# Optimization experiments

Hardware: AMD Instinct MI355X
Metric: run time of the kernel (lower is better)

The kernel has to match this reference:

```python
import jax, jax.numpy as jnp
import numpy as np

N_NODES = 100000
N_EDGES = 1600000
F_IN = 128
HID = 64
N_CLS = 40


def _sage_conv(x, src, dst, Wl, bl, Wr, num_nodes):
    # PyG SAGEConv (aggr='mean', root_weight=True, normalize=False):
    # out = lin_l(mean_{j in N(i)} x_j) + lin_r(x_i)
    msg = x[src]                                              # [E, F] gather
    agg = jax.ops.segment_sum(msg, dst, num_segments=num_nodes)
    deg = jax.ops.segment_sum(jnp.ones_like(dst, dtype=x.dtype), dst,
                              num_segments=num_nodes)
    mean = agg / jnp.maximum(deg, 1.0)[:, None]               # [N, F]
    return mean @ Wl.T + bl + x @ Wr.T


def setup_inputs() -> dict:
    key = jax.random.key(0)
    ks = jax.random.split(key, 16)

    def lin(k, out_d, in_d):
        bound = 1.0 / np.sqrt(in_d)
        return jax.random.uniform(k, (out_d, in_d), jnp.float32, -bound, bound)

    x = jax.random.normal(ks[0], (N_NODES, F_IN), jnp.float32)
    edge_index = jax.random.randint(ks[1], (2, N_EDGES), 0, N_NODES, jnp.int64)

    return {
        "x": x,
        "edge_index": edge_index,
        "W1l": lin(ks[2], HID, F_IN), "b1": jnp.zeros((HID,), jnp.float32),
        "W1r": lin(ks[3], HID, F_IN),
        "W2l": lin(ks[4], HID, HID), "b2": jnp.zeros((HID,), jnp.float32),
        "W2r": lin(ks[5], HID, HID),
        "W3l": lin(ks[6], HID, HID), "b3": jnp.zeros((HID,), jnp.float32),
        "W3r": lin(ks[7], HID, HID),
        "Wout": lin(ks[8], N_CLS, HID),
        "bout": jnp.zeros((N_CLS,), jnp.float32),
    }


def reference(x, edge_index, W1l, b1, W1r, W2l, b2, W2r, W3l, b3, W3r, Wout, bout):
    src, dst = edge_index[0], edge_index[1]
    n = x.shape[0]
    h = _sage_conv(x, src, dst, W1l, b1, W1r, n)
    h = jax.nn.elu(h)
    h = _sage_conv(h, src, dst, W2l, b2, W2r, n)
    h = jax.nn.elu(h)
    h = _sage_conv(h, src, dst, W3l, b3, W3r, n)
    return h @ Wout.T + bout
```

## Files before the change

kernel.cpp:

```cpp
#include <hip/hip_runtime.h>


static inline size_t ws_align(size_t x) { return (x + 511) & ~size_t(511); }

#define MAXBC  104
#define CAPL   96
#define EB_CAP 24576

using frag_ab = __attribute__((ext_vector_type(8))) short;
using f32x4   = __attribute__((ext_vector_type(4))) float;
using us4     = __attribute__((ext_vector_type(4))) unsigned short;

__device__ inline short f2bf(float f) {
    unsigned u = __builtin_bit_cast(unsigned, f);
    u += 0x7fff + ((u >> 16) & 1);
    return (short)(u >> 16);
}
__device__ inline float b2f(unsigned short h) {
    unsigned u = ((unsigned)h) << 16;
    return __builtin_bit_cast(float, u);
}


__global__ void zero_kernel(int* __restrict__ p, int n) {
    int i = blockIdx.x * blockDim.x + threadIdx.x;
    if (i < n) p[i] = 0;
}

__global__ void prep_all(const float* __restrict__ W1l, const float* __restrict__ W1r,
                         const float* __restrict__ W2l, const float* __restrict__ W2r,
                         const float* __restrict__ W3l, const float* __restrict__ W3r,
                         unsigned short* __restrict__ fw) {
    const int idx = blockIdx.x * 256 + threadIdx.x;
    if (idx >= 32768) return;
    const float* W;
    unsigned short* out;
    int F, rel;
    if (idx < 8192)       { W = W1l; out = fw;        F = 128; rel = idx; }
    else if (idx < 16384) { W = W1r; out = fw + 8192; F = 128; rel = idx - 8192; }
    else {
        const int q = (idx - 16384) >> 12;
        rel = (idx - 16384) & 4095;
        F = 64;
        W = (q == 0) ? W2l : (q == 1) ? W2r : (q == 2) ? W3l : W3r;
        out = fw + 16384 + q * 4096;
    }
    const int k = rel % F;
    const int col = rel / F;
    out[(k >> 3) * 512 + col * 8 + (k & 7)] = (unsigned short)f2bf(W[rel]);
}


__global__ void pass1_bin(const int* __restrict__ src, const int* __restrict__ dst,
                          int* __restrict__ bcur, unsigned* __restrict__ ebuf,
                          int nE, int nN, int nbc) {
    __shared__ unsigned lbuf[MAXBC][CAPL];
    __shared__ int bcnt[MAXBC];
    __shared__ int gbase[MAXBC];
    const int t = threadIdx.x;
    const int e0 = blockIdx.x * 4096;
    for (int i = t; i < MAXBC; i += 256) bcnt[i] = 0;
    __syncthreads();
#pragma unroll
    for (int q = 0; q < 16; ++q) {
        const int e = e0 + q * 256 + t;
        if (e < nE) {
            const unsigned d = (unsigned)dst[e];
            const unsigned s = (unsigned)src[e];
            if (d < (unsigned)nN && s < (unsigned)nN) {
                const int cb = (int)(d >> 10);
                const unsigned v = ((d & 1023u) << 17) | s;
                const int pos = atomicAdd(&bcnt[cb], 1);
                if (pos < CAPL) {
                    lbuf[cb][pos] = v;
                } else {
                    const int gp = atomicAdd(&bcur[cb], 1);
                    if (gp < EB_CAP) ebuf[(size_t)cb * EB_CAP + gp] = v;
                }
            }
        }
    }
    __syncthreads();
    for (int b = t; b < nbc; b += 256) {
        const int cnt = min(bcnt[b], CAPL);
        bcnt[b] = cnt;
        gbase[b] = (cnt > 0) ? atomicAdd(&bcur[b], cnt) : 0;
    }
    __syncthreads();
    const int wid = t >> 6, lane = t & 63;
    for (int b = wid; b < nbc; b += 4) {
        const int cnt = bcnt[b];
        const int gb = gbase[b];
        for (int i = lane; i < cnt; i += 64) {
            const int gp = gb + i;
            if (gp < EB_CAP) ebuf[(size_t)b * EB_CAP + gp] = lbuf[b][i];
        }
    }
}

__global__ void scan_buckets(const int* __restrict__ bcur, int* __restrict__ bbase, int nbc) {
    __shared__ int sdata[256];
    const int t = threadIdx.x;
    const int v = (t < nbc) ? min(bcur[t], EB_CAP) : 0;
    sdata[t] = v;
    __syncthreads();
    for (int off = 1; off < 256; off <<= 1) {
        int add = (t >= off) ? sdata[t - off] : 0;
        __syncthreads();
        sdata[t] += add;
        __syncthreads();
    }
    if (t < nbc) bbase[t] = sdata[t] - v;
}

__global__ void pass2_build(const unsigned* __restrict__ ebuf,
                            const int* __restrict__ bcur, const int* __restrict__ bbase,
                            int* __restrict__ rowptr, int* __restrict__ csr,
                            int nN, int nbc) {
    __shared__ int lcnt[1024];
    __shared__ int lcur[1024];
    __shared__ int sdata[256];
    const int b = blockIdx.x;
    const int node0 = b << 10;
    const int nloc = min(1024, nN - node0);
    if (nloc <= 0) return;
    const int cnt  = min(bcur[b], EB_CAP);
    const int base = bbase[b];
    const int t = threadIdx.x;
    const unsigned* eb = ebuf + (size_t)b * EB_CAP;

    for (int i = t; i < 1024; i += 256) lcnt[i] = 0;
    __syncthreads();
    for (int i = t; i < cnt; i += 256) atomicAdd(&lcnt[eb[i] >> 17], 1);
    __syncthreads();
    int v[4];
    int tsum = 0;
#pragma unroll
    for (int q = 0; q < 4; ++q) { v[q] = lcnt[t * 4 + q]; tsum += v[q]; }
    sdata[t] = tsum;
    __syncthreads();
    for (int off = 1; off < 256; off <<= 1) {
        int add = (t >= off) ? sdata[t - off] : 0;
        __syncthreads();
        sdata[t] += add;
        __syncthreads();
    }
    int run = sdata[t] - tsum;
#pragma unroll
    for (int q = 0; q < 4; ++q) {
        const int l = t * 4 + q;
        lcur[l] = run;
        if (l < nloc) rowptr[node0 + l] = base + run;
        run += v[q];
    }
    if (b == nbc - 1 && t == 0) rowptr[nN] = base + cnt;
    __syncthreads();
    for (int i = t; i < cnt; i += 256) {
        const unsigned ev = eb[i];
        const int pos = atomicAdd(&lcur[ev >> 17], 1);
        csr[base + pos] = (int)(ev & 0x1FFFFu);
    }
}

template<int F, bool AF32>
__global__ void proj2_mfma(const void* __restrict__ Aptr,
                           const unsigned short* __restrict__ fwl,
                           const unsigned short* __restrict__ fwr,
                           const float* __restrict__ bias,
                           unsigned short* __restrict__ xl,
                           float* __restrict__ xr,
                           int nN) {
    const int t    = threadIdx.x;
    const int wave = t >> 6;
    const int lane = t & 63;
    const int lg   = lane >> 4;
    const int lr   = lane & 15;
    const int row0 = blockIdx.x * 64 + wave * 16;

    const float*          Af = (const float*)Aptr;
    const unsigned short* Ab = (const unsigned short*)Aptr;

    f32x4 accl[4] = {};
    f32x4 accr[4] = {};

#pragma unroll
    for (int ks = 0; ks < F / 32; ++ks) {
        const int k0 = ks * 32 + lg * 8;
        frag_ab afr;
        {
            int row = row0 + lr;
            if (row >= nN) row = nN - 1;
            if constexpr (AF32) {
                const float4 f0 = *reinterpret_cast<const float4*>(Af + (size_t)row * F + k0);
                const float4 f1 = *reinterpret_cast<const float4*>(Af + (size_t)row * F + k0 + 4);
                afr[0] = f2bf(f0.x); afr[1] = f2bf(f0.y); afr[2] = f2bf(f0.z); afr[3] = f2bf(f0.w);
                afr[4] = f2bf(f1.x); afr[5] = f2bf(f1.y); afr[6] = f2bf(f1.z); afr[7] = f2bf(f1.w);
            } else {
                afr = *reinterpret_cast<const frag_ab*>(Ab + (size_t)row * F + k0);
            }
        }
        const int ob = (ks * 4 + lg) * 512;
#pragma unroll
        for (int nf = 0; nf < 4; ++nf) {
            const int col = nf * 16 + lr;
            const frag_ab bl = *reinterpret_cast<const frag_ab*>(fwl + ob + col * 8);
            const frag_ab br = *reinterpret_cast<const frag_ab*>(fwr + ob + col * 8);
            accl[nf] = __builtin_amdgcn_mfma_f32_16x16x32_bf16(afr, bl, accl[nf], 0, 0, 0);
            accr[nf] = __builtin_amdgcn_mfma_f32_16x16x32_bf16(afr, br, accr[nf], 0, 0, 0);
        }
    }

#pragma unroll
    for (int nf = 0; nf < 4; ++nf) {
        const int col = nf * 16 + lr;
        const float bv = bias[col];
#pragma unroll
        for (int j = 0; j < 4; ++j) {
            const int row = row0 + lg * 4 + j;
            if (row < nN) {
                xl[(size_t)row * 64 + col] = (unsigned short)f2bf(accl[nf][j]);
                xr[(size_t)row * 64 + col] = accr[nf][j] + bv;
            }
        }
    }
}

template<bool DOELU>
__global__ void gather_kernel(const unsigned short* __restrict__ xl,
                              const float* __restrict__ xr,
                              const int* __restrict__ rowptr, const int* __restrict__ csr,
                              unsigned short* __restrict__ outp, int nN, int nE) {
    const int node = blockIdx.x * (blockDim.x >> 6) + (threadIdx.x >> 6);
    if (node >= nN) return;
    const int lane = threadIdx.x & 63;
    const unsigned loff = (unsigned)(lane << 1);
    int b = rowptr[node];
    int e = rowptr[node + 1];
    b = max(0, min(b, nE));
    e = max(b, min(e, nE));
    const float d = (float)(e - b);
    const char* xlb = (const char*)xl;

    float acc = 0.f;
    int i = b;
    for (; i + 16 <= e; i += 16) {
        const int iv = csr[i + (lane & 15)];
        unsigned short v[16];
#pragma unroll
        for (int j = 0; j < 16; ++j) {
            const unsigned s = (unsigned)__shfl(iv, j);
            v[j] = *(const unsigned short*)(xlb + (s * 128u + loff));
        }
#pragma unroll
        for (int j = 0; j < 16; ++j) acc += b2f(v[j]);
    }
    if (i < e) {
        const int lim = e - i;
        const int iv = csr[i + min(lane & 15, lim - 1)];
        unsigned short v[16];
#pragma unroll
        for (int j = 0; j < 16; ++j) {
            const unsigned s = (unsigned)__shfl(iv, j);
            v[j] = *(const unsigned short*)(xlb + (s * 128u + loff));
        }
#pragma unroll
        for (int j = 0; j < 16; ++j) acc += (j < lim) ? b2f(v[j]) : 0.f;
    }

    float vout = acc / fmaxf(d, 1.0f) + xr[(size_t)node * 64 + lane];
    if (DOELU) vout = vout > 0.f ? vout : expm1f(vout);
    outp[(size_t)node * 64 + lane] = (unsigned short)f2bf(vout);
}

template<int F, int NOUT>
__global__ void head_kernel(const unsigned short* __restrict__ A,
                            const float* __restrict__ W,
                            const float* __restrict__ bias,
                            float* __restrict__ out, int nN) {
    constexpr int NCH = F / 32;
    __shared__ float As[64][36];
    __shared__ float Bs[32][64];

    const int t = threadIdx.x;
    const int block0 = blockIdx.x * 64;
    const int tm = (t >> 4) << 2;
    const int tn = (t & 15) << 2;

    float acc[4][4] = {};

    for (int ch = 0; ch < NCH; ++ch) {
        const int kg0 = ch * 32;
        {
            const int kk = (t & 7) * 4;
#pragma unroll
            for (int r = 0; r < 2; ++r) {
                const int n = (t >> 3) + r * 32;
                const int node = block0 + n;
                float4 v = make_float4(0.f, 0.f, 0.f, 0.f);
                if (node < nN) {
                    const us4 u = *reinterpret_cast<const us4*>(A + (size_t)node * F + kg0 + kk);
                    v.x = b2f(u[0]); v.y = b2f(u[1]); v.z = b2f(u[2]); v.w = b2f(u[3]);
                }
                *reinterpret_cast<float4*>(&As[n][kk]) = v;
            }
        }
        {
            const int j = t & 63;
#pragma unroll
            for (int p = 0; p < 8; ++p) {
                const int kk = (t >> 6) + p * 4;
                Bs[kk][j] = (j < NOUT) ? W[(size_t)j * F + kg0 + kk] : 0.0f;
            }
        }
        __syncthreads();
#pragma unroll
        for (int kk = 0; kk < 32; ++kk) {
            const float a0 = As[tm + 0][kk];
            const float a1 = As[tm + 1][kk];
            const float a2 = As[tm + 2][kk];
            const float a3 = As[tm + 3][kk];
            const float4 bv = *reinterpret_cast<const float4*>(&Bs[kk][tn]);
            acc[0][0] += a0 * bv.x; acc[0][1] += a0 * bv.y; acc[0][2] += a0 * bv.z; acc[0][3] += a0 * bv.w;
            acc[1][0] += a1 * bv.x; acc[1][1] += a1 * bv.y; acc[1][2] += a1 * bv.z; acc[1][3] += a1 * bv.w;
            acc[2][0] += a2 * bv.x; acc[2][1] += a2 * bv.y; acc[2][2] += a2 * bv.z; acc[2][3] += a2 * bv.w;
            acc[3][0] += a3 * bv.x; acc[3][1] += a3 * bv.y; acc[3][2] += a3 * bv.z; acc[3][3] += a3 * bv.w;
        }
        __syncthreads();
    }

#pragma unroll
    for (int i = 0; i < 4; ++i) {
        const int node = block0 + tm + i;
        if (node >= nN) continue;
#pragma unroll
        for (int j = 0; j < 4; ++j) {
            const int col = tn + j;
            if (col < NOUT)
                out[(size_t)node * NOUT + col] = acc[i][j] + bias[col];
        }
    }
}


extern "C" void kernel_launch(void* const* d_in, const int* in_sizes, int n_in,
                              void* d_out, int out_size, void* d_ws, size_t ws_size,
                              hipStream_t stream) {
    const float* x    = (const float*)d_in[0];
    const int*   ei   = (const int*)d_in[1];
    const float* W1l  = (const float*)d_in[2];
    const float* b1   = (const float*)d_in[3];
    const float* W1r  = (const float*)d_in[4];
    const float* W2l  = (const float*)d_in[5];
    const float* b2   = (const float*)d_in[6];
    const float* W2r  = (const float*)d_in[7];
    const float* W3l  = (const float*)d_in[8];
    const float* b3   = (const float*)d_in[9];
    const float* W3r  = (const float*)d_in[10];
    const float* Wout = (const float*)d_in[11];
    const float* bout = (const float*)d_in[12];

    const int N = in_sizes[0] / 128;
    const int E = in_sizes[1] / 2;
    const int* src  = ei;
    const int* dstA = ei + E;
    const int nbc = (N + 1023) >> 10;

    char* ws = (char*)d_ws;
    size_t o = 0;
    int* bcur    = (int*)(ws + o); o += ws_align((size_t)MAXBC * 4);
    int* bbase   = (int*)(ws + o); o += ws_align((size_t)MAXBC * 4);
    int* rowptr  = (int*)(ws + o); o += ws_align((size_t)(N + 1) * 4);
    int* csr     = (int*)(ws + o); o += ws_align((size_t)E * 4);
    unsigned* ebuf = (unsigned*)(ws + o); o += ws_align((size_t)MAXBC * EB_CAP * 4);
    unsigned short* fw  = (unsigned short*)(ws + o); o += ws_align((size_t)32768 * 2);
    unsigned short* xl  = (unsigned short*)(ws + o); o += ws_align((size_t)N * 64 * 2);
    float*          xr  = (float*)(ws + o);          o += ws_align((size_t)N * 64 * 4);
    unsigned short* hAb = (unsigned short*)(ws + o); o += ws_align((size_t)N * 64 * 2);
    unsigned short* hBb = (unsigned short*)(ws + o); o += ws_align((size_t)N * 64 * 2);
    unsigned short* h3b = (unsigned short*)(ws + o); o += ws_align((size_t)N * 64 * 2);
    float* outp = (float*)d_out;

    const int projGrid = (N + 63) / 64;
    const int gatherGrid = (N + 3) / 4;
    const int headGrid = (N + 63) / 64;

    zero_kernel<<<1, 256, 0, stream>>>(bcur, MAXBC);
    prep_all<<<128, 256, 0, stream>>>(W1l, W1r, W2l, W2r, W3l, W3r, fw);
    pass1_bin<<<(E + 4095) / 4096, 256, 0, stream>>>(src, dstA, bcur, ebuf, E, N, nbc);
    scan_buckets<<<1, 256, 0, stream>>>(bcur, bbase, nbc);
    pass2_build<<<nbc, 256, 0, stream>>>(ebuf, bcur, bbase, rowptr, csr, N, nbc);

    const unsigned short* fw1l = fw;
    const unsigned short* fw1r = fw + 8192;
    const unsigned short* fw2l = fw + 16384;
    const unsigned short* fw2r = fw + 16384 + 4096;
    const unsigned short* fw3l = fw + 16384 + 8192;
    const unsigned short* fw3r = fw + 16384 + 12288;

    proj2_mfma<128, true><<<projGrid, 256, 0, stream>>>(x, fw1l, fw1r, b1, xl, xr, N);
    gather_kernel<true><<<gatherGrid, 256, 0, stream>>>(xl, xr, rowptr, csr, hAb, N, E);

    proj2_mfma<64, false><<<projGrid, 256, 0, stream>>>(hAb, fw2l, fw2r, b2, xl, xr, N);
    gather_kernel<true><<<gatherGrid, 256, 0, stream>>>(xl, xr, rowptr, csr, hBb, N, E);

    proj2_mfma<64, false><<<projGrid, 256, 0, stream>>>(hBb, fw3l, fw3r, b3, xl, xr, N);
    gather_kernel<false><<<gatherGrid, 256, 0, stream>>>(xl, xr, rowptr, csr, h3b, N, E);

    head_kernel<64, 40><<<headGrid, 256, 0, stream>>>(h3b, Wout, bout, outp, N);
}
```

Baseline: 276.8 us.

## Vectorize neighbor gather with 16-byte loads and cross-lane reduction

The gather kernel now has each lane load 16 bytes (8 bf16 features) of a neighbor row, so a wave covers 8 neighbors per load instead of one 2-byte element per lane per neighbor. Partial sums are reduced across lane groups with xor shuffles, and one group of 8 lanes writes the result with vector stores. The CSR array now stores byte offsets (index<<7), which removes a multiply per load. This cuts load instruction count and raises memory-level parallelism, at the cost of shuffle reductions and only 8 active lanes in the epilogue.

```diff
diff --git a/kernel.cpp b/kernel.cpp
--- a/kernel.cpp
+++ b/kernel.cpp
@@ -20,6 +20,8 @@
     unsigned u = ((unsigned)h) << 16;
     return __builtin_bit_cast(float, u);
 }
+__device__ inline float bflo(unsigned u) { return __builtin_bit_cast(float, u << 16); }
+__device__ inline float bfhi(unsigned u) { return __builtin_bit_cast(float, u & 0xffff0000u); }
 
 
 __global__ void zero_kernel(int* __restrict__ p, int n) {
@@ -158,7 +160,7 @@
     for (int i = t; i < cnt; i += 256) {
         const unsigned ev = eb[i];
         const int pos = atomicAdd(&lcur[ev >> 17], 1);
-        csr[base + pos] = (int)(ev & 0x1FFFFu);
+        csr[base + pos] = (int)((ev & 0x1FFFFu) << 7);
     }
 }
 
@@ -233,7 +235,9 @@
     const int node = blockIdx.x * (blockDim.x >> 6) + (threadIdx.x >> 6);
     if (node >= nN) return;
     const int lane = threadIdx.x & 63;
-    const unsigned loff = (unsigned)(lane << 1);
+    const int fg = lane & 7;
+    const int rs = lane >> 3;
+    const unsigned fgo = (unsigned)(fg << 4);
     int b = rowptr[node];
     int e = rowptr[node + 1];
     b = max(0, min(b, nE));
@@ -241,35 +245,69 @@
     const float d = (float)(e - b);
     const char* xlb = (const char*)xl;
 
-    float acc = 0.f;
+    float acc[8] = {};
     int i = b;
     for (; i + 16 <= e; i += 16) {
         const int iv = csr[i + (lane & 15)];
-        unsigned short v[16];
-#pragma unroll
-        for (int j = 0; j < 16; ++j) {
-            const unsigned s = (unsigned)__shfl(iv, j);
-            v[j] = *(const unsigned short*)(xlb + (s * 128u + loff));
-        }
-#pragma unroll
-        for (int j = 0; j < 16; ++j) acc += b2f(v[j]);
+        const int s0 = __shfl(iv, rs);
+        const int s1 = __shfl(iv, 8 + rs);
+        const uint4 u0 = *reinterpret_cast<const uint4*>(xlb + ((unsigned)s0 + fgo));
+        const uint4 u1 = *reinterpret_cast<const uint4*>(xlb + ((unsigned)s1 + fgo));
+        acc[0] += bflo(u0.x); acc[1] += bfhi(u0.x);
+        acc[2] += bflo(u0.y); acc[3] += bfhi(u0.y);
+        acc[4] += bflo(u0.z); acc[5] += bfhi(u0.z);
+        acc[6] += bflo(u0.w); acc[7] += bfhi(u0.w);
+        acc[0] += bflo(u1.x); acc[1] += bfhi(u1.x);
+        acc[2] += bflo(u1.y); acc[3] += bfhi(u1.y);
+        acc[4] += bflo(u1.z); acc[5] += bfhi(u1.z);
+        acc[6] += bflo(u1.w); acc[7] += bfhi(u1.w);
     }
     if (i < e) {
         const int lim = e - i;
         const int iv = csr[i + min(lane & 15, lim - 1)];
-        unsigned short v[16];
-#pragma unroll
-        for (int j = 0; j < 16; ++j) {
-            const unsigned s = (unsigned)__shfl(iv, j);
-            v[j] = *(const unsigned short*)(xlb + (s * 128u + loff));
-        }
-#pragma unroll
-        for (int j = 0; j < 16; ++j) acc += (j < lim) ? b2f(v[j]) : 0.f;
-    }
-
-    float vout = acc / fmaxf(d, 1.0f) + xr[(size_t)node * 64 + lane];
-    if (DOELU) vout = vout > 0.f ? vout : expm1f(vout);
-    outp[(size_t)node * 64 + lane] = (unsigned short)f2bf(vout);
+        const int s0 = __shfl(iv, min(rs, lim - 1));
+        const int s1 = __shfl(iv, min(8 + rs, lim - 1));
+        uint4 u0 = *reinterpret_cast<const uint4*>(xlb + ((unsigned)s0 + fgo));
+        uint4 u1 = *reinterpret_cast<const uint4*>(xlb + ((unsigned)s1 + fgo));
+        if (rs >= lim)     { u0.x = 0u; u0.y = 0u; u0.z = 0u; u0.w = 0u; }
+        if (8 + rs >= lim) { u1.x = 0u; u1.y = 0u; u1.z = 0u; u1.w = 0u; }
+        acc[0] += bflo(u0.x); acc[1] += bfhi(u0.x);
+        acc[2] += bflo(u0.y); acc[3] += bfhi(u0.y);
+        acc[4] += bflo(u0.z); acc[5] += bfhi(u0.z);
+        acc[6] += bflo(u0.w); acc[7] += bfhi(u0.w);
+        acc[0] += bflo(u1.x); acc[1] += bfhi(u1.x);
+        acc[2] += bflo(u1.y); acc[3] += bfhi(u1.y);
+        acc[4] += bflo(u1.z); acc[5] += bfhi(u1.z);
+        acc[6] += bflo(u1.w); acc[7] += bfhi(u1.w);
+    }
+
+#pragma unroll
+    for (int k = 0; k < 8; ++k) acc[k] += __shfl_xor(acc[k], 8);
+#pragma unroll
+    for (int k = 0; k < 8; ++k) acc[k] += __shfl_xor(acc[k], 16);
+#pragma unroll
+    for (int k = 0; k < 8; ++k) acc[k] += __shfl_xor(acc[k], 32);
+
+    if (rs == 0) {
+        const float inv = 1.0f / fmaxf(d, 1.0f);
+        const float4 r0 = *reinterpret_cast<const float4*>(xr + (size_t)node * 64 + fg * 8);
+        const float4 r1 = *reinterpret_cast<const float4*>(xr + (size_t)node * 64 + fg * 8 + 4);
+        float v[8];
+        v[0] = acc[0] * inv + r0.x; v[1] = acc[1] * inv + r0.y;
+        v[2] = acc[2] * inv + r0.z; v[3] = acc[3] * inv + r0.w;
+        v[4] = acc[4] * inv + r1.x; v[5] = acc[5] * inv + r1.y;
+        v[6] = acc[6] * inv + r1.z; v[7] = acc[7] * inv + r1.w;
+        if (DOELU) {
+#pragma unroll
+            for (int k = 0; k < 8; ++k) v[k] = v[k] > 0.f ? v[k] : expm1f(v[k]);
+        }
+        uint4 p;
+        p.x = ((unsigned)(unsigned short)f2bf(v[0])) | (((unsigned)(unsigned short)f2bf(v[1])) << 16);
+        p.y = ((unsigned)(unsigned short)f2bf(v[2])) | (((unsigned)(unsigned short)f2bf(v[3])) << 16);
+        p.z = ((unsigned)(unsigned short)f2bf(v[4])) | (((unsigned)(unsigned short)f2bf(v[5])) << 16);
+        p.w = ((unsigned)(unsigned short)f2bf(v[6])) | (((unsigned)(unsigned short)f2bf(v[7])) << 16);
+        *reinterpret_cast<uint4*>(outp + (size_t)node * 64 + fg * 8) = p;
+    }
 }
 
 template<int F, int NOUT>
```

New measurement: 298.5 us. +7.8%, slower.
